# Kernel tuning notes

Measured on AMD Instinct MI355X. Metric: run time of the kernel, lower is better.

Reference implementation:

```python
import jax, jax.numpy as jnp
import numpy as np

N = 100000
E = 800000
IN_DIM = 256
HEADS = 8
OUT_DIM = 32
OUT_ALL = HEADS * OUT_DIM  # 256 == IN_DIM -> residual is Identity
NEG_SLOPE = 0.2


def setup_inputs() -> dict:
    key = jax.random.key(0)
    ks = jax.random.split(key, 10)
    s_in = 1.0 / np.sqrt(IN_DIM)
    x = jax.random.normal(ks[0], (N, IN_DIM), dtype=jnp.float32)
    edge_index = jax.random.randint(ks[1], (2, E), 0, N, dtype=jnp.int64)
    Wl = jax.random.normal(ks[2], (IN_DIM, OUT_ALL), dtype=jnp.float32) * s_in
    bl = jnp.zeros((OUT_ALL,), dtype=jnp.float32)
    Wr = jax.random.normal(ks[3], (IN_DIM, OUT_ALL), dtype=jnp.float32) * s_in
    br = jnp.zeros((OUT_ALL,), dtype=jnp.float32)
    att = jax.random.normal(ks[4], (HEADS, OUT_DIM), dtype=jnp.float32) * (1.0 / np.sqrt(OUT_DIM))
    bias = jnp.zeros((OUT_ALL,), dtype=jnp.float32)
    gamma = jnp.ones((OUT_ALL,), dtype=jnp.float32)
    beta = jnp.zeros((OUT_ALL,), dtype=jnp.float32)
    return {"x": x, "edge_index": edge_index, "Wl": Wl, "bl": bl, "Wr": Wr,
            "br": br, "att": att, "bias": bias, "gamma": gamma, "beta": beta}


def reference(x, edge_index, Wl, bl, Wr, br, att, bias, gamma, beta):
    src, dst = edge_index[0], edge_index[1]
    # GATv2: separate transforms for source (lin_l) and target (lin_r)
    x_l = (x @ Wl + bl).reshape(N, HEADS, OUT_DIM)  # messages / source side
    x_r = (x @ Wr + br).reshape(N, HEADS, OUT_DIM)  # target side
    # edge-wise GATv2 score: a^T LeakyReLU(x_j + x_i)
    s = jax.nn.leaky_relu(x_l[src] + x_r[dst], NEG_SLOPE)  # [E, H, D]
    e = jnp.einsum('ehd,hd->eh', s, att)                   # [E, H]
    # segment softmax over incoming edges of each destination node
    m = jax.ops.segment_max(e, dst, num_segments=N)        # [N, H]
    p = jnp.exp(e - m[dst])                                # [E, H]
    denom = jax.ops.segment_sum(p, dst, num_segments=N)    # [N, H]
    denom = jnp.where(denom == 0, 1.0, denom)
    alpha = p / denom[dst]                                 # [E, H]
    # scatter-sum aggregate of alpha * lin_l(x_src)
    msg = alpha[:, :, None] * x_l[src]                     # [E, H, D]
    out = jax.ops.segment_sum(msg, dst, num_segments=N)    # [N, H, D]
    y = out.reshape(N, OUT_ALL) + bias
    # residual is Identity since in_dim == heads*out_dim
    z = y + x
    # LayerNorm then ELU
    mu = jnp.mean(z, axis=-1, keepdims=True)
    var = jnp.var(z, axis=-1, keepdims=True)
    zn = (z - mu) * jax.lax.rsqrt(var + 1e-5) * gamma + beta
    return jax.nn.elu(zn)
```

## Files before the change

### kernel.cpp

```cpp
#include <hip/hip_runtime.h>
#include <hip/hip_bf16.h>

#define NN 100000
#define EE 800000
#define DALL 256
#define NEG 0.2f

typedef __attribute__((ext_vector_type(8))) short bf16x8;
typedef __attribute__((ext_vector_type(4))) float f32x4;

static __device__ __forceinline__ ushort f2b(float f) {
    __hip_bfloat16 h = __float2bfloat16(f);
    return *reinterpret_cast<ushort*>(&h);
}
static __device__ __forceinline__ float b2f(ushort u) {
    union { float f; unsigned v; } c; c.v = ((unsigned)u) << 16; return c.f;
}
static __device__ __forceinline__ void unpack8(uint4 u, float* v) {
    v[0] = b2f((ushort)(u.x & 0xffff)); v[1] = b2f((ushort)(u.x >> 16));
    v[2] = b2f((ushort)(u.y & 0xffff)); v[3] = b2f((ushort)(u.y >> 16));
    v[4] = b2f((ushort)(u.z & 0xffff)); v[5] = b2f((ushort)(u.z >> 16));
    v[6] = b2f((ushort)(u.w & 0xffff)); v[7] = b2f((ushort)(u.w >> 16));
}

__global__ __launch_bounds__(256) void cvt_x(const float* __restrict__ in,
                                             ushort* __restrict__ out)
{
    const int total = NN * DALL / 8;
    for (int i = blockIdx.x * 256 + threadIdx.x; i < total; i += gridDim.x * 256) {
        float4 a = reinterpret_cast<const float4*>(in)[i * 2];
        float4 b = reinterpret_cast<const float4*>(in)[i * 2 + 1];
        uint4 o;
        o.x = f2b(a.x) | ((unsigned)f2b(a.y) << 16);
        o.y = f2b(a.z) | ((unsigned)f2b(a.w) << 16);
        o.z = f2b(b.x) | ((unsigned)f2b(b.y) << 16);
        o.w = f2b(b.z) | ((unsigned)f2b(b.w) << 16);
        reinterpret_cast<uint4*>(out)[i] = o;
    }
}

__global__ __launch_bounds__(256) void cvt_W(const float* __restrict__ Wl,
                                             const float* __restrict__ Wr,
                                             ushort* __restrict__ Wt)
{
    __shared__ float tile[32][33];
    int kt = blockIdx.x * 32, nt = blockIdx.y * 32;
    int tx = threadIdx.x & 31, ty = threadIdx.x >> 5;
#pragma unroll
    for (int i = 0; i < 32; i += 8) {
        int k = kt + ty + i, n = nt + tx;
        float v = (n < 256) ? Wl[(size_t)k * 256 + n] : Wr[(size_t)k * 256 + (n - 256)];
        tile[ty + i][tx] = v;
    }
    __syncthreads();
#pragma unroll
    for (int i = 0; i < 32; i += 8) {
        int n = nt + ty + i, k = kt + tx;
        Wt[(size_t)n * 256 + k] = f2b(tile[tx][ty + i]);
    }
}

__global__ __launch_bounds__(256) void gemm_dual(
    const ushort* __restrict__ xb,
    const ushort* __restrict__ Wt,
    const float* __restrict__ bl, const float* __restrict__ br,
    ushort* __restrict__ xl, ushort* __restrict__ xr)
{
    __shared__ __align__(16) ushort smem[2][2][128 * 32];

    const int bx = blockIdx.x;
    const int rowBase = (bx >> 2) * 128;
    const int colBase = (bx & 3) * 128;
    const int t = threadIdx.x, lane = t & 63, wave = t >> 6;
    const int wr = (wave >> 1) * 64, wc = (wave & 1) * 64;

    const int sr  = lane >> 2;
    const int sc8 = (lane & 3) * 8;

    f32x4 acc[4][4];
#pragma unroll
    for (int m = 0; m < 4; ++m)
#pragma unroll
        for (int n = 0; n < 4; ++n) acc[m][n] = (f32x4){0.f, 0.f, 0.f, 0.f};

    auto STAGE = [&](int buf, int kb) {
#pragma unroll
        for (int tt = 0; tt < 2; ++tt) {
            int rbase = wave * 32 + tt * 16;
            int r = rbase + sr;
            int ga = rowBase + r; if (ga >= NN) ga = NN - 1;
            const ushort* gpA = xb + (size_t)ga * 256 + kb + sc8;
            ushort* lpA = &smem[buf][0][rbase * 32];
            __builtin_amdgcn_global_load_lds(
                (const __attribute__((address_space(1))) unsigned int*)gpA,
                (__attribute__((address_space(3))) unsigned int*)lpA, 16, 0, 0);
            int gb = colBase + r;
            const ushort* gpB = Wt + (size_t)gb * 256 + kb + sc8;
            ushort* lpB = &smem[buf][1][rbase * 32];
            __builtin_amdgcn_global_load_lds(
                (const __attribute__((address_space(1))) unsigned int*)gpB,
                (__attribute__((address_space(3))) unsigned int*)lpB, 16, 0, 0);
        }
    };

    STAGE(0, 0);
    __syncthreads();

#pragma unroll
    for (int s = 0; s < 8; ++s) {
        if (s < 7) STAGE((s + 1) & 1, (s + 1) * 32);
        const ushort* A = smem[s & 1][0];
        const ushort* B = smem[s & 1][1];
        bf16x8 af[4], bfr[4];
#pragma unroll
        for (int m = 0; m < 4; ++m)
            af[m] = *reinterpret_cast<const bf16x8*>(
                &A[(wr + m * 16 + (lane & 15)) * 32 + (lane >> 4) * 8]);
#pragma unroll
        for (int n = 0; n < 4; ++n)
            bfr[n] = *reinterpret_cast<const bf16x8*>(
                &B[(wc + n * 16 + (lane & 15)) * 32 + (lane >> 4) * 8]);
#pragma unroll
        for (int m = 0; m < 4; ++m)
#pragma unroll
            for (int n = 0; n < 4; ++n)
                acc[m][n] = __builtin_amdgcn_mfma_f32_16x16x32_bf16(
                    af[m], bfr[n], acc[m][n], 0, 0, 0);
        if (s < 7) __syncthreads();
    }

    const bool isL = (colBase < 256);
    ushort* OutP = isL ? xl : xr;
    const float* bvp = isL ? bl : br;
    const int cb0 = colBase & 255;

    int colLoc[4]; float bb[4];
#pragma unroll
    for (int n = 0; n < 4; ++n) {
        colLoc[n] = cb0 + wc + n * 16 + (lane & 15);
        bb[n] = bvp[colLoc[n]];
    }
#pragma unroll
    for (int m = 0; m < 4; ++m) {
        int r0 = rowBase + wr + m * 16 + (lane >> 4) * 4;
#pragma unroll
        for (int r = 0; r < 4; ++r) {
            int row = r0 + r;
            if (row < NN) {
#pragma unroll
                for (int n = 0; n < 4; ++n)
                    OutP[(size_t)row * 256 + colLoc[n]] = f2b(acc[m][n][r] + bb[n]);
            }
        }
    }
}

__global__ __launch_bounds__(256) void count_deg(const int* __restrict__ dst,
                                                 int* __restrict__ cnt)
{
    int e = blockIdx.x * 256 + threadIdx.x;
    if (e < EE) atomicAdd(&cnt[dst[e]], 1);
}

__global__ __launch_bounds__(256) void scan_part1(const int* __restrict__ cnt,
                                                  int* __restrict__ bsums)
{
    __shared__ int red[256];
    int base = blockIdx.x * 1024 + threadIdx.x * 4;
    int s = 0;
#pragma unroll
    for (int k = 0; k < 4; ++k) { int i = base + k; if (i < NN) s += cnt[i]; }
    red[threadIdx.x] = s; __syncthreads();
    for (int off = 128; off > 0; off >>= 1) {
        if (threadIdx.x < off) red[threadIdx.x] += red[threadIdx.x + off];
        __syncthreads();
    }
    if (threadIdx.x == 0) bsums[blockIdx.x] = red[0];
}

__global__ void scan_part2(int* bsums, int nb, int* rowptr)
{
    if (threadIdx.x == 0 && blockIdx.x == 0) {
        int run = 0;
        for (int i = 0; i < nb; ++i) { int v = bsums[i]; bsums[i] = run; run += v; }
        rowptr[NN] = run;
    }
}

__global__ __launch_bounds__(256) void scan_part3(const int* __restrict__ cnt,
                                                  const int* __restrict__ bsums,
                                                  int* __restrict__ rowptr)
{
    __shared__ int pre[256];
    int base = blockIdx.x * 1024 + threadIdx.x * 4;
    int v[4]; int s = 0;
#pragma unroll
    for (int k = 0; k < 4; ++k) { int i = base + k; v[k] = (i < NN) ? cnt[i] : 0; s += v[k]; }
    pre[threadIdx.x] = s; __syncthreads();
    for (int off = 1; off < 256; off <<= 1) {
        int tv = (threadIdx.x >= off) ? pre[threadIdx.x - off] : 0;
        __syncthreads();
        pre[threadIdx.x] += tv;
        __syncthreads();
    }
    int excl = pre[threadIdx.x] - s + bsums[blockIdx.x];
#pragma unroll
    for (int k = 0; k < 4; ++k) {
        int i = base + k;
        if (i < NN) { rowptr[i] = excl; excl += v[k]; }
    }
}

__global__ __launch_bounds__(256) void fill_csr(const int* __restrict__ src,
                                                const int* __restrict__ dst,
                                                const int* __restrict__ rowptr,
                                                int* __restrict__ cursor,
                                                int* __restrict__ srcs)
{
    int e = blockIdx.x * 256 + threadIdx.x;
    if (e >= EE) return;
    int d = dst[e];
    int pos = atomicAdd(&cursor[d], 1);
    srcs[rowptr[d] + pos] = src[e];
}

__global__ __launch_bounds__(256) void aggregate_finalize(
    const ushort* __restrict__ xl, const ushort* __restrict__ xr,
    const int* __restrict__ srcs, const int* __restrict__ rowptr,
    const float* __restrict__ att, const ushort* __restrict__ xb,
    const float* __restrict__ bias, const float* __restrict__ gamma,
    const float* __restrict__ beta, float* __restrict__ out)
{
    int node = blockIdx.x * 4 + (threadIdx.x >> 6);
    if (node >= NN) return;
    int lane = threadIdx.x & 63;
    int half = lane >> 5;
    int dl = lane & 31;
    const int off = dl * 8;

    uint4 xru = *reinterpret_cast<const uint4*>(xr + (size_t)node * DALL + off);
    float xrv[8]; unpack8(xru, xrv);
    float atv[8];
    {
        float4 a0 = *reinterpret_cast<const float4*>(att + off);
        float4 a1 = *reinterpret_cast<const float4*>(att + off + 4);
        atv[0]=a0.x; atv[1]=a0.y; atv[2]=a0.z; atv[3]=a0.w;
        atv[4]=a1.x; atv[5]=a1.y; atv[6]=a1.z; atv[7]=a1.w;
    }

    int beg = rowptr[node], end = rowptr[node + 1];
    float a[8] = {0.f,0.f,0.f,0.f,0.f,0.f,0.f,0.f};
    float dsum = 0.f;

    for (int base = beg; base < end; base += 4) {
        int jA = base + half;
        int jB = base + 2 + half;
        bool vA = jA < end, vB = jB < end;
        int sA = srcs[vA ? jA : beg];
        int sB = srcs[vB ? jB : beg];
        uint4 gA = *reinterpret_cast<const uint4*>(xl + (size_t)sA * DALL + off);
        uint4 gB = *reinterpret_cast<const uint4*>(xl + (size_t)sB * DALL + off);
        float vAv[8], vBv[8]; unpack8(gA, vAv); unpack8(gB, vBv);
        float pA = 0.f, pB = 0.f;
#pragma unroll
        for (int i = 0; i < 8; ++i) {
            float z = vAv[i] + xrv[i];
            z = fmaxf(z, 0.f) + NEG * fminf(z, 0.f);
            pA += z * atv[i];
            float z2 = vBv[i] + xrv[i];
            z2 = fmaxf(z2, 0.f) + NEG * fminf(z2, 0.f);
            pB += z2 * atv[i];
        }
        pA += __shfl_xor(pA, 1); pA += __shfl_xor(pA, 2);
        pB += __shfl_xor(pB, 1); pB += __shfl_xor(pB, 2);
        float peA = vA ? __expf(pA) : 0.f;
        float peB = vB ? __expf(pB) : 0.f;
#pragma unroll
        for (int i = 0; i < 8; ++i) a[i] += peA * vAv[i] + peB * vBv[i];
        dsum += peA + peB;
    }

#pragma unroll
    for (int i = 0; i < 8; ++i) a[i] += __shfl_xor(a[i], 32);
    dsum += __shfl_xor(dsum, 32);
    float inv = dsum > 0.f ? 1.f / dsum : 0.f;

    uint4 xbu = *reinterpret_cast<const uint4*>(xb + (size_t)node * DALL + off);
    float xv[8]; unpack8(xbu, xv);
    float bvv[8], gvv[8], bev[8];
    {
        float4 b0 = *reinterpret_cast<const float4*>(bias + off);
        float4 b1 = *reinterpret_cast<const float4*>(bias + off + 4);
        bvv[0]=b0.x; bvv[1]=b0.y; bvv[2]=b0.z; bvv[3]=b0.w;
        bvv[4]=b1.x; bvv[5]=b1.y; bvv[6]=b1.z; bvv[7]=b1.w;
        float4 g0 = *reinterpret_cast<const float4*>(gamma + off);
        float4 g1 = *reinterpret_cast<const float4*>(gamma + off + 4);
        gvv[0]=g0.x; gvv[1]=g0.y; gvv[2]=g0.z; gvv[3]=g0.w;
        gvv[4]=g1.x; gvv[5]=g1.y; gvv[6]=g1.z; gvv[7]=g1.w;
        float4 e0 = *reinterpret_cast<const float4*>(beta + off);
        float4 e1 = *reinterpret_cast<const float4*>(beta + off + 4);
        bev[0]=e0.x; bev[1]=e0.y; bev[2]=e0.z; bev[3]=e0.w;
        bev[4]=e1.x; bev[5]=e1.y; bev[6]=e1.z; bev[7]=e1.w;
    }

    float y[8]; float sum = 0.f, sq = 0.f;
#pragma unroll
    for (int i = 0; i < 8; ++i) {
        y[i] = a[i] * inv + bvv[i] + xv[i];
        sum += y[i]; sq += y[i] * y[i];
    }
#pragma unroll
    for (int m = 1; m < 32; m <<= 1) {
        sum += __shfl_xor(sum, m);
        sq  += __shfl_xor(sq, m);
    }
    float mu  = sum * (1.0f / 256.0f);
    float var = sq * (1.0f / 256.0f) - mu * mu;
    float rr  = rsqrtf(var + 1e-5f);

    if (half == 0) {
        float4 o0, o1;
        float z0 = (y[0]-mu)*rr*gvv[0] + bev[0];
        float z1 = (y[1]-mu)*rr*gvv[1] + bev[1];
        float z2 = (y[2]-mu)*rr*gvv[2] + bev[2];
        float z3 = (y[3]-mu)*rr*gvv[3] + bev[3];
        float z4 = (y[4]-mu)*rr*gvv[4] + bev[4];
        float z5 = (y[5]-mu)*rr*gvv[5] + bev[5];
        float z6 = (y[6]-mu)*rr*gvv[6] + bev[6];
        float z7 = (y[7]-mu)*rr*gvv[7] + bev[7];
        o0.x = z0 > 0.f ? z0 : expm1f(z0);
        o0.y = z1 > 0.f ? z1 : expm1f(z1);
        o0.z = z2 > 0.f ? z2 : expm1f(z2);
        o0.w = z3 > 0.f ? z3 : expm1f(z3);
        o1.x = z4 > 0.f ? z4 : expm1f(z4);
        o1.y = z5 > 0.f ? z5 : expm1f(z5);
        o1.z = z6 > 0.f ? z6 : expm1f(z6);
        o1.w = z7 > 0.f ? z7 : expm1f(z7);
        *reinterpret_cast<float4*>(out + (size_t)node * DALL + off)     = o0;
        *reinterpret_cast<float4*>(out + (size_t)node * DALL + off + 4) = o1;
    }
}

extern "C" void kernel_launch(void* const* d_in, const int* in_sizes, int n_in,
                              void* d_out, int out_size, void* d_ws, size_t ws_size,
                              hipStream_t stream)
{
    const float* x    = (const float*)d_in[0];
    const int*   edge = (const int*)d_in[1];
    const float* Wl   = (const float*)d_in[2];
    const float* bl   = (const float*)d_in[3];
    const float* Wr   = (const float*)d_in[4];
    const float* br   = (const float*)d_in[5];
    const float* att  = (const float*)d_in[6];
    const float* bias = (const float*)d_in[7];
    const float* gamma= (const float*)d_in[8];
    const float* beta = (const float*)d_in[9];
    float* out = (float*)d_out;

    const int* srcIdx = edge;
    const int* dstIdx = edge + EE;

    ushort* xl = (ushort*)d_ws;
    ushort* xr = xl + (size_t)NN * DALL;
    ushort* xb = xr + (size_t)NN * DALL;
    ushort* Wt = xb + (size_t)NN * DALL;
    int* rowptr = (int*)(Wt + 512 * 256);
    int* cursor = rowptr + NN + 1;
    int* srcs   = cursor + NN;
    int* bsums  = srcs + EE;

    const int SCAN_NB = (NN + 1023) / 1024;

    cvt_x<<<2048, 256, 0, stream>>>(x, xb);
    cvt_W<<<dim3(8, 16), 256, 0, stream>>>(Wl, Wr, Wt);
    gemm_dual<<<782 * 4, 256, 0, stream>>>(xb, Wt, bl, br, xl, xr);

    hipMemsetAsync(cursor, 0, NN * sizeof(int), stream);
    count_deg<<<(EE + 255) / 256, 256, 0, stream>>>(dstIdx, cursor);
    scan_part1<<<SCAN_NB, 256, 0, stream>>>(cursor, bsums);
    scan_part2<<<1, 64, 0, stream>>>(bsums, SCAN_NB, rowptr);
    scan_part3<<<SCAN_NB, 256, 0, stream>>>(cursor, bsums, rowptr);
    hipMemsetAsync(cursor, 0, NN * sizeof(int), stream);
    fill_csr<<<(EE + 255) / 256, 256, 0, stream>>>(srcIdx, dstIdx, rowptr, cursor, srcs);

    aggregate_finalize<<<NN / 4, 256, 0, stream>>>(
        xl, xr, srcs, rowptr, att, xb, bias, gamma, beta, out);
}
```

Baseline: 305.7 us.

## Fuse preprocessing kernels, simplify CSR build, unroll aggregation over four edges

Merges the x and weight bf16 conversions and the degree count into one kernel launch. The separate scan_part2 is folded into the row-pointer scan, where each block reduces the preceding block sums itself. fill_csr now uses the row pointer array as its atomic cursor, which removes a memset and a read, and after filling the entries shift so that node n's range runs from rowptr[n-1] to rowptr[n]. The aggregation loop processes eight edges per iteration instead of four to expose more independent gathers, at the cost of more registers.

```diff
diff --git a/kernel.cpp b/kernel.cpp
--- a/kernel.cpp
+++ b/kernel.cpp
@@ -5,6 +5,10 @@
 #define EE 800000
 #define DALL 256
 #define NEG 0.2f
+
+#define CNT_BLOCKS 3125
+#define CVTW_BLOCKS 128
+#define CVTX_BLOCKS 2048
 
 typedef __attribute__((ext_vector_type(8))) short bf16x8;
 typedef __attribute__((ext_vector_type(4))) float f32x4;
@@ -23,40 +27,47 @@
     v[6] = b2f((ushort)(u.w & 0xffff)); v[7] = b2f((ushort)(u.w >> 16));
 }
 
-__global__ __launch_bounds__(256) void cvt_x(const float* __restrict__ in,
-                                             ushort* __restrict__ out)
-{
+__global__ __launch_bounds__(256) void fused_init(
+    const float* __restrict__ x, const float* __restrict__ Wl,
+    const float* __restrict__ Wr, const int* __restrict__ dst,
+    ushort* __restrict__ xb, ushort* __restrict__ Wt, int* __restrict__ cnt)
+{
+    __shared__ float tile[32][33];
+    int b = blockIdx.x;
+    if (b < CNT_BLOCKS) {
+        int e = b * 256 + threadIdx.x;
+        if (e < EE) atomicAdd(&cnt[dst[e]], 1);
+        return;
+    }
+    b -= CNT_BLOCKS;
+    if (b < CVTW_BLOCKS) {
+        int kt = (b & 7) * 32, nt = (b >> 3) * 32;
+        int tx = threadIdx.x & 31, ty = threadIdx.x >> 5;
+#pragma unroll
+        for (int i = 0; i < 32; i += 8) {
+            int k = kt + ty + i, n = nt + tx;
+            float v = (n < 256) ? Wl[(size_t)k * 256 + n] : Wr[(size_t)k * 256 + (n - 256)];
+            tile[ty + i][tx] = v;
+        }
+        __syncthreads();
+#pragma unroll
+        for (int i = 0; i < 32; i += 8) {
+            int n = nt + ty + i, k = kt + tx;
+            Wt[(size_t)n * 256 + k] = f2b(tile[tx][ty + i]);
+        }
+        return;
+    }
+    b -= CVTW_BLOCKS;
     const int total = NN * DALL / 8;
-    for (int i = blockIdx.x * 256 + threadIdx.x; i < total; i += gridDim.x * 256) {
-        float4 a = reinterpret_cast<const float4*>(in)[i * 2];
-        float4 b = reinterpret_cast<const float4*>(in)[i * 2 + 1];
+    for (int i = b * 256 + threadIdx.x; i < total; i += CVTX_BLOCKS * 256) {
+        float4 a = reinterpret_cast<const float4*>(x)[i * 2];
+        float4 c = reinterpret_cast<const float4*>(x)[i * 2 + 1];
         uint4 o;
         o.x = f2b(a.x) | ((unsigned)f2b(a.y) << 16);
         o.y = f2b(a.z) | ((unsigned)f2b(a.w) << 16);
-        o.z = f2b(b.x) | ((unsigned)f2b(b.y) << 16);
-        o.w = f2b(b.z) | ((unsigned)f2b(b.w) << 16);
-        reinterpret_cast<uint4*>(out)[i] = o;
-    }
-}
-
-__global__ __launch_bounds__(256) void cvt_W(const float* __restrict__ Wl,
-                                             const float* __restrict__ Wr,
-                                             ushort* __restrict__ Wt)
-{
-    __shared__ float tile[32][33];
-    int kt = blockIdx.x * 32, nt = blockIdx.y * 32;
-    int tx = threadIdx.x & 31, ty = threadIdx.x >> 5;
-#pragma unroll
-    for (int i = 0; i < 32; i += 8) {
-        int k = kt + ty + i, n = nt + tx;
-        float v = (n < 256) ? Wl[(size_t)k * 256 + n] : Wr[(size_t)k * 256 + (n - 256)];
-        tile[ty + i][tx] = v;
-    }
-    __syncthreads();
-#pragma unroll
-    for (int i = 0; i < 32; i += 8) {
-        int n = nt + ty + i, k = kt + tx;
-        Wt[(size_t)n * 256 + k] = f2b(tile[tx][ty + i]);
+        o.z = f2b(c.x) | ((unsigned)f2b(c.y) << 16);
+        o.w = f2b(c.z) | ((unsigned)f2b(c.w) << 16);
+        reinterpret_cast<uint4*>(xb)[i] = o;
     }
 }
 
@@ -155,13 +166,6 @@
     }
 }
 
-__global__ __launch_bounds__(256) void count_deg(const int* __restrict__ dst,
-                                                 int* __restrict__ cnt)
-{
-    int e = blockIdx.x * 256 + threadIdx.x;
-    if (e < EE) atomicAdd(&cnt[dst[e]], 1);
-}
-
 __global__ __launch_bounds__(256) void scan_part1(const int* __restrict__ cnt,
                                                   int* __restrict__ bsums)
 {
@@ -178,32 +182,33 @@
     if (threadIdx.x == 0) bsums[blockIdx.x] = red[0];
 }
 
-__global__ void scan_part2(int* bsums, int nb, int* rowptr)
-{
-    if (threadIdx.x == 0 && blockIdx.x == 0) {
-        int run = 0;
-        for (int i = 0; i < nb; ++i) { int v = bsums[i]; bsums[i] = run; run += v; }
-        rowptr[NN] = run;
-    }
-}
-
-__global__ __launch_bounds__(256) void scan_part3(const int* __restrict__ cnt,
-                                                  const int* __restrict__ bsums,
-                                                  int* __restrict__ rowptr)
-{
+__global__ __launch_bounds__(256) void scan_rowptr(const int* __restrict__ cnt,
+                                                   const int* __restrict__ bsums,
+                                                   int* __restrict__ rowptr)
+{
+    __shared__ int redB[256];
     __shared__ int pre[256];
-    int base = blockIdx.x * 1024 + threadIdx.x * 4;
+    int tb = threadIdx.x;
+    redB[tb] = (tb < (int)blockIdx.x) ? bsums[tb] : 0;
+    __syncthreads();
+    for (int off = 128; off > 0; off >>= 1) {
+        if (tb < off) redB[tb] += redB[tb + off];
+        __syncthreads();
+    }
+    int base0 = redB[0];
+
+    int base = blockIdx.x * 1024 + tb * 4;
     int v[4]; int s = 0;
 #pragma unroll
     for (int k = 0; k < 4; ++k) { int i = base + k; v[k] = (i < NN) ? cnt[i] : 0; s += v[k]; }
-    pre[threadIdx.x] = s; __syncthreads();
+    pre[tb] = s; __syncthreads();
     for (int off = 1; off < 256; off <<= 1) {
-        int tv = (threadIdx.x >= off) ? pre[threadIdx.x - off] : 0;
-        __syncthreads();
-        pre[threadIdx.x] += tv;
-        __syncthreads();
-    }
-    int excl = pre[threadIdx.x] - s + bsums[blockIdx.x];
+        int tv = (tb >= off) ? pre[tb - off] : 0;
+        __syncthreads();
+        pre[tb] += tv;
+        __syncthreads();
+    }
+    int excl = pre[tb] - s + base0;
 #pragma unroll
     for (int k = 0; k < 4; ++k) {
         int i = base + k;
@@ -213,15 +218,13 @@
 
 __global__ __launch_bounds__(256) void fill_csr(const int* __restrict__ src,
                                                 const int* __restrict__ dst,
-                                                const int* __restrict__ rowptr,
-                                                int* __restrict__ cursor,
+                                                int* __restrict__ rowptr,
                                                 int* __restrict__ srcs)
 {
     int e = blockIdx.x * 256 + threadIdx.x;
     if (e >= EE) return;
-    int d = dst[e];
-    int pos = atomicAdd(&cursor[d], 1);
-    srcs[rowptr[d] + pos] = src[e];
+    int pos = atomicAdd(&rowptr[dst[e]], 1);
+    srcs[pos] = src[e];
 }
 
 __global__ __launch_bounds__(256) void aggregate_finalize(
@@ -248,36 +251,47 @@
         atv[4]=a1.x; atv[5]=a1.y; atv[6]=a1.z; atv[7]=a1.w;
     }
 
-    int beg = rowptr[node], end = rowptr[node + 1];
+    int beg = node ? rowptr[node - 1] : 0;
+    int end = rowptr[node];
     float a[8] = {0.f,0.f,0.f,0.f,0.f,0.f,0.f,0.f};
     float dsum = 0.f;
 
-    for (int base = beg; base < end; base += 4) {
-        int jA = base + half;
-        int jB = base + 2 + half;
-        bool vA = jA < end, vB = jB < end;
-        int sA = srcs[vA ? jA : beg];
-        int sB = srcs[vB ? jB : beg];
-        uint4 gA = *reinterpret_cast<const uint4*>(xl + (size_t)sA * DALL + off);
-        uint4 gB = *reinterpret_cast<const uint4*>(xl + (size_t)sB * DALL + off);
-        float vAv[8], vBv[8]; unpack8(gA, vAv); unpack8(gB, vBv);
-        float pA = 0.f, pB = 0.f;
+    for (int base = beg; base < end; base += 8) {
+        int j0 = base + half;
+        int j1 = base + 2 + half;
+        int j2 = base + 4 + half;
+        int j3 = base + 6 + half;
+        bool k0 = j0 < end, k1 = j1 < end, k2 = j2 < end, k3 = j3 < end;
+        int s0 = srcs[k0 ? j0 : beg];
+        int s1 = srcs[k1 ? j1 : beg];
+        int s2 = srcs[k2 ? j2 : beg];
+        int s3 = srcs[k3 ? j3 : beg];
+        uint4 g0 = *reinterpret_cast<const uint4*>(xl + (size_t)s0 * DALL + off);
+        uint4 g1 = *reinterpret_cast<const uint4*>(xl + (size_t)s1 * DALL + off);
+        uint4 g2 = *reinterpret_cast<const uint4*>(xl + (size_t)s2 * DALL + off);
+        uint4 g3 = *reinterpret_cast<const uint4*>(xl + (size_t)s3 * DALL + off);
+        float v0v[8], v1v[8], v2v[8], v3v[8];
+        unpack8(g0, v0v); unpack8(g1, v1v); unpack8(g2, v2v); unpack8(g3, v3v);
+        float p0 = 0.f, p1 = 0.f, p2 = 0.f, p3 = 0.f;
 #pragma unroll
         for (int i = 0; i < 8; ++i) {
-            float z = vAv[i] + xrv[i];
-            z = fmaxf(z, 0.f) + NEG * fminf(z, 0.f);
-            pA += z * atv[i];
-            float z2 = vBv[i] + xrv[i];
-            z2 = fmaxf(z2, 0.f) + NEG * fminf(z2, 0.f);
-            pB += z2 * atv[i];
-        }
-        pA += __shfl_xor(pA, 1); pA += __shfl_xor(pA, 2);
-        pB += __shfl_xor(pB, 1); pB += __shfl_xor(pB, 2);
-        float peA = vA ? __expf(pA) : 0.f;
-        float peB = vB ? __expf(pB) : 0.f;
-#pragma unroll
-        for (int i = 0; i < 8; ++i) a[i] += peA * vAv[i] + peB * vBv[i];
-        dsum += peA + peB;
+            float z0 = v0v[i] + xrv[i]; p0 += fmaxf(z0, NEG * z0) * atv[i];
+            float z1 = v1v[i] + xrv[i]; p1 += fmaxf(z1, NEG * z1) * atv[i];
+            float z2 = v2v[i] + xrv[i]; p2 += fmaxf(z2, NEG * z2) * atv[i];
+            float z3 = v3v[i] + xrv[i]; p3 += fmaxf(z3, NEG * z3) * atv[i];
+        }
+        p0 += __shfl_xor(p0, 1); p0 += __shfl_xor(p0, 2);
+        p1 += __shfl_xor(p1, 1); p1 += __shfl_xor(p1, 2);
+        p2 += __shfl_xor(p2, 1); p2 += __shfl_xor(p2, 2);
+        p3 += __shfl_xor(p3, 1); p3 += __shfl_xor(p3, 2);
+        float e0 = k0 ? __expf(p0) : 0.f;
+        float e1 = k1 ? __expf(p1) : 0.f;
+        float e2 = k2 ? __expf(p2) : 0.f;
+        float e3 = k3 ? __expf(p3) : 0.f;
+#pragma unroll
+        for (int i = 0; i < 8; ++i)
+            a[i] += e0 * v0v[i] + e1 * v1v[i] + e2 * v2v[i] + e3 * v3v[i];
+        dsum += e0 + e1 + e2 + e3;
     }
 
 #pragma unroll
@@ -365,24 +379,19 @@
     ushort* xb = xr + (size_t)NN * DALL;
     ushort* Wt = xb + (size_t)NN * DALL;
     int* rowptr = (int*)(Wt + 512 * 256);
-    int* cursor = rowptr + NN + 1;
-    int* srcs   = cursor + NN;
+    int* cnt    = rowptr + NN + 1;
+    int* srcs   = cnt + NN;
     int* bsums  = srcs + EE;
 
     const int SCAN_NB = (NN + 1023) / 1024;
 
-    cvt_x<<<2048, 256, 0, stream>>>(x, xb);
-    cvt_W<<<dim3(8, 16), 256, 0, stream>>>(Wl, Wr, Wt);
+    hipMemsetAsync(cnt, 0, NN * sizeof(int), stream);
+    fused_init<<<CNT_BLOCKS + CVTW_BLOCKS + CVTX_BLOCKS, 256, 0, stream>>>(
+        x, Wl, Wr, dstIdx, xb, Wt, cnt);
     gemm_dual<<<782 * 4, 256, 0, stream>>>(xb, Wt, bl, br, xl, xr);
-
-    hipMemsetAsync(cursor, 0, NN * sizeof(int), stream);
-    count_deg<<<(EE + 255) / 256, 256, 0, stream>>>(dstIdx, cursor);
-    scan_part1<<<SCAN_NB, 256, 0, stream>>>(cursor, bsums);
-    scan_part2<<<1, 64, 0, stream>>>(bsums, SCAN_NB, rowptr);
-    scan_part3<<<SCAN_NB, 256, 0, stream>>>(cursor, bsums, rowptr);
-    hipMemsetAsync(cursor, 0, NN * sizeof(int), stream);
-    fill_csr<<<(EE + 255) / 256, 256, 0, stream>>>(srcIdx, dstIdx, rowptr, cursor, srcs);
-
+    scan_part1<<<SCAN_NB, 256, 0, stream>>>(cnt, bsums);
+    scan_rowptr<<<SCAN_NB, 256, 0, stream>>>(cnt, bsums, rowptr);
+    fill_csr<<<(EE + 255) / 256, 256, 0, stream>>>(srcIdx, dstIdx, rowptr, srcs);
     aggregate_finalize<<<NN / 4, 256, 0, stream>>>(
         xl, xr, srcs, rowptr, att, xb, bias, gamma, beta, out);
 }
```

New measurement: 306.3 us. Within noise of the previous version (+0.2%).
